# Optimization experiments

Hardware: AMD Instinct MI355X
Metric: run time of the kernel (lower is better)

Reference implementation:

```python
import jax, jax.numpy as jnp
import numpy as np

H, W = 768, 1024
N_ITER = 10
DIST_THR = 100.0 / 15.0
NORMAL_THR = 0.34
DAMP = 1e-9  # tiny ridge so the 6x6 normal-equation solve matches lstsq robustly


def _skew(w):
    z = jnp.zeros((), w.dtype)
    return jnp.stack([
        jnp.stack([z, -w[2], w[1]]),
        jnp.stack([w[2], z, -w[0]]),
        jnp.stack([-w[1], w[0], z]),
    ])


def _so3_exp(w):
    # Rodrigues formula, safe at w ~ 0
    th2 = jnp.dot(w, w)
    th = jnp.sqrt(th2 + 1e-12)
    Wm = _skew(w)
    return (jnp.eye(3, dtype=w.dtype)
            + (jnp.sin(th) / th) * Wm
            + ((1.0 - jnp.cos(th)) / (th2 + 1e-12)) * (Wm @ Wm))


def _pose(x):
    # lie_se3_to_SE3: rotation = exp(x[:3]), translation = x[3:]
    return _so3_exp(x[:3]), x[3:]


def _backproject(depth, K):
    # PointCloud.from_depth: grid_pts[v,u] = depth[v,u] * K^-1 @ [u, v, 1]
    vs, us = jnp.meshgrid(jnp.arange(H, dtype=depth.dtype),
                          jnp.arange(W, dtype=depth.dtype), indexing='ij')
    Kinv = jnp.linalg.inv(K)
    uv1 = jnp.stack([us, vs, jnp.ones_like(us)], axis=-1)  # [H,W,3]
    return (uv1 @ Kinv.T) * depth[..., None]               # [H,W,3]


def _grid_normals(pts):
    # normals from cross product of image-space gradients of the 3D grid
    du = jnp.gradient(pts, axis=1)
    dv = jnp.gradient(pts, axis=0)
    n = jnp.cross(du, dv)
    return n / jnp.sqrt(jnp.sum(n * n, axis=-1, keepdims=True) + 1e-12)


def _icp(ref_depth, target_pts, target_normals, K):
    dt = ref_depth.dtype
    ref_grid = _backproject(ref_depth, K)   # [H,W,3]
    ref_nrm = _grid_normals(ref_grid)       # [H,W,3]
    x = jnp.zeros(6, dtype=dt)
    cost = jnp.zeros((), dtype=dt)
    for _ in range(N_ITER):
        R, t = _pose(x)
        # transform target cloud into current ref camera frame: inv(T) @ p
        pts_c = (target_pts - t) @ R        # R^T (p - t), [N,3]
        nrm_c = target_normals @ R          # rotate normals by R^T
        # projective association
        uvw = pts_c @ K.T
        z = uvw[:, 2]
        zs = jnp.where(jnp.abs(z) > 1e-8, z, 1e-8)
        u = uvw[:, 0] / zs
        v = uvw[:, 1] / zs
        valid = (u > 0) & (u < W) & (v > 0) & (v < H) & (z > 1e-6)
        iu = jnp.clip(u, 0, W - 1).astype(jnp.int32)
        iv = jnp.clip(v, 0, H - 1).astype(jnp.int32)
        rg = ref_grid[iv, iu]               # gathered ref grid points [N,3]
        rn = ref_nrm[iv, iu]                # gathered ref grid normals [N,3]
        dist = jnp.sqrt(jnp.sum((rg - pts_c) ** 2, axis=-1) + 1e-12)
        valid = valid & (dist < DIST_THR) & (jnp.sum(rn * nrm_c, axis=-1) > NORMAL_THR)
        w = valid.astype(dt)
        # point-to-plane residual in world/target frame: n_trg . (T @ p_ref - p_trg)
        ref_world = rg @ R.T + t
        r = jnp.sum(target_normals * (ref_world - target_pts), axis=-1) * w
        # J row = n^T @ j_3d(p) = [cross(p, n), n]
        J = jnp.concatenate([jnp.cross(ref_world, target_normals), target_normals], axis=-1) * w[:, None]
        cost = jnp.sum(r * r) / jnp.maximum(jnp.sum(w), 1.0)
        A = J.T @ J + DAMP * jnp.eye(6, dtype=dt)
        x = x - jnp.linalg.solve(A, J.T @ r)  # Gauss-Newton step (= -lstsq(J, r))
    Rf, tf = _pose(x)
    T = jnp.eye(4, dtype=dt).at[:3, :3].set(Rf).at[:3, 3].set(tf)
    return T, cost


def setup_inputs() -> dict:
    key = jax.random.key(0)
    k1, k2 = jax.random.split(key)
    K = jnp.array([[1000.0, 0.0, 512.0],
                   [0.0, 1000.0, 384.0],
                   [0.0, 0.0, 1.0]], dtype=jnp.float32)
    vs, us = jnp.meshgrid(jnp.arange(H, dtype=jnp.float32),
                          jnp.arange(W, dtype=jnp.float32), indexing='ij')
    base = 1.0 + 0.2 * jnp.sin(vs / 47.0) * jnp.cos(us / 53.0)  # smooth surface
    ref_depth = (base + 0.001 * jax.random.normal(k1, (H, W))).astype(jnp.float32)
    trg_depth = (base + 0.001 * jax.random.normal(k2, (H, W))).astype(jnp.float32)
    tg = _backproject(trg_depth, K)
    tn = _grid_normals(tg)
    return {
        'ref_depth': ref_depth,
        'target_pts': tg.reshape(-1, 3),
        'target_normals': tn.reshape(-1, 3),
        'intrinsics': K,
    }


def reference(ref_depth, target_pts, target_normals, intrinsics):
    return _icp(ref_depth, target_pts, target_normals, intrinsics)
```

## Files before the change

kernel.cpp:

```cpp
#include <hip/hip_runtime.h>
#include <math.h>

#define H_IMG 768
#define W_IMG 1024
#define NPTS (H_IMG * W_IMG)
#define NITER 10
#define DIST_THR (100.0f / 15.0f)
#define NORMAL_THR 0.34f

struct Ctrl {
    double accum[NITER][32];
    double x[6];
    float  pose[NITER + 1][12];
    float  Kinv[9];
};

__global__ void setup_kernel(const float* __restrict__ K, Ctrl* c) {
    int tid = threadIdx.x;
    double* ac = &c->accum[0][0];
    for (int i = tid; i < NITER * 32; i += blockDim.x) ac[i] = 0.0;
    if (tid < 6) c->x[tid] = 0.0;
    if (tid == 0) {
        float* p0 = c->pose[0];
        p0[0] = 1.f; p0[1] = 0.f; p0[2] = 0.f;
        p0[3] = 0.f; p0[4] = 1.f; p0[5] = 0.f;
        p0[6] = 0.f; p0[7] = 0.f; p0[8] = 1.f;
        p0[9] = 0.f; p0[10] = 0.f; p0[11] = 0.f;
        double a = K[0], b = K[1], cc = K[2];
        double d = K[3], e = K[4], f = K[5];
        double g = K[6], h = K[7], i = K[8];
        double det = a * (e * i - f * h) - b * (d * i - f * g) + cc * (d * h - e * g);
        double idet = 1.0 / det;
        c->Kinv[0] = (float)((e * i - f * h) * idet);
        c->Kinv[1] = (float)((cc * h - b * i) * idet);
        c->Kinv[2] = (float)((b * f - cc * e) * idet);
        c->Kinv[3] = (float)((f * g - d * i) * idet);
        c->Kinv[4] = (float)((a * i - cc * g) * idet);
        c->Kinv[5] = (float)((cc * d - a * f) * idet);
        c->Kinv[6] = (float)((d * h - e * g) * idet);
        c->Kinv[7] = (float)((b * g - a * h) * idet);
        c->Kinv[8] = (float)((a * e - b * d) * idet);
    }
}

__global__ __launch_bounds__(256) void backproject_kernel(const float* __restrict__ depth,
                                                          const Ctrl* __restrict__ c,
                                                          float* __restrict__ grid) {
    int i = blockIdx.x * blockDim.x + threadIdx.x;
    if (i >= NPTS) return;
    int v = i >> 10;
    int u = i & 1023;
    float d = depth[i];
    float uf = (float)u, vf = (float)v;
    const float* Ki = c->Kinv;
    grid[3 * i + 0] = (Ki[0] * uf + Ki[1] * vf + Ki[2]) * d;
    grid[3 * i + 1] = (Ki[3] * uf + Ki[4] * vf + Ki[5]) * d;
    grid[3 * i + 2] = (Ki[6] * uf + Ki[7] * vf + Ki[8]) * d;
}

__global__ __launch_bounds__(256) void normals_kernel(const float* __restrict__ grid,
                                                      float* __restrict__ nrm) {
    int i = blockIdx.x * blockDim.x + threadIdx.x;
    if (i >= NPTS) return;
    int v = i >> 10;
    int u = i & 1023;
    int um = (u > 0) ? u - 1 : 0;
    int up = (u < W_IMG - 1) ? u + 1 : W_IMG - 1;
    int vm = (v > 0) ? v - 1 : 0;
    int vp = (v < H_IMG - 1) ? v + 1 : H_IMG - 1;
    float su = (u > 0 && u < W_IMG - 1) ? 0.5f : 1.0f;
    float sv = (v > 0 && v < H_IMG - 1) ? 0.5f : 1.0f;
    int il = (v * W_IMG + um) * 3, ir = (v * W_IMG + up) * 3;
    int it = (vm * W_IMG + u) * 3, ib = (vp * W_IMG + u) * 3;
    float dux = (grid[ir + 0] - grid[il + 0]) * su;
    float duy = (grid[ir + 1] - grid[il + 1]) * su;
    float duz = (grid[ir + 2] - grid[il + 2]) * su;
    float dvx = (grid[ib + 0] - grid[it + 0]) * sv;
    float dvy = (grid[ib + 1] - grid[it + 1]) * sv;
    float dvz = (grid[ib + 2] - grid[it + 2]) * sv;
    float nx = duy * dvz - duz * dvy;
    float ny = duz * dvx - dux * dvz;
    float nz = dux * dvy - duy * dvx;
    float len = sqrtf(nx * nx + ny * ny + nz * nz + 1e-12f);
    nrm[3 * i + 0] = nx / len;
    nrm[3 * i + 1] = ny / len;
    nrm[3 * i + 2] = nz / len;
}

__global__ __launch_bounds__(256) void icp_main(const float* __restrict__ tp,
                                                const float* __restrict__ tn,
                                                const float* __restrict__ grid,
                                                const float* __restrict__ nrm,
                                                const float* __restrict__ K,
                                                const float* __restrict__ pose,
                                                double* __restrict__ accum) {
    const float R0 = pose[0], R1 = pose[1], R2 = pose[2];
    const float R3 = pose[3], R4 = pose[4], R5 = pose[5];
    const float R6 = pose[6], R7 = pose[7], R8 = pose[8];
    const float t0 = pose[9], t1 = pose[10], t2 = pose[11];
    const float K0 = K[0], K1 = K[1], K2 = K[2];
    const float K3 = K[3], K4 = K[4], K5 = K[5];
    const float K6 = K[6], K7 = K[7], K8 = K[8];

    float acc[29];
#pragma unroll
    for (int k = 0; k < 29; ++k) acc[k] = 0.f;

    const int stride = gridDim.x * blockDim.x;
    for (int i = blockIdx.x * blockDim.x + threadIdx.x; i < NPTS; i += stride) {
        float p0 = tp[3 * i + 0], p1 = tp[3 * i + 1], p2 = tp[3 * i + 2];
        float n0 = tn[3 * i + 0], n1 = tn[3 * i + 1], n2 = tn[3 * i + 2];
        float d0 = p0 - t0, d1 = p1 - t1, d2 = p2 - t2;
        float pc0 = R0 * d0 + R3 * d1 + R6 * d2;
        float pc1 = R1 * d0 + R4 * d1 + R7 * d2;
        float pc2 = R2 * d0 + R5 * d1 + R8 * d2;
        float nc0 = R0 * n0 + R3 * n1 + R6 * n2;
        float nc1 = R1 * n0 + R4 * n1 + R7 * n2;
        float nc2 = R2 * n0 + R5 * n1 + R8 * n2;
        float uu = K0 * pc0 + K1 * pc1 + K2 * pc2;
        float vv = K3 * pc0 + K4 * pc1 + K5 * pc2;
        float zz = K6 * pc0 + K7 * pc1 + K8 * pc2;
        float zs = (fabsf(zz) > 1e-8f) ? zz : 1e-8f;
        float uf = uu / zs, vf = vv / zs;
        bool valid = (uf > 0.f) && (uf < (float)W_IMG) && (vf > 0.f) && (vf < (float)H_IMG) && (zz > 1e-6f);
        int iu = (int)fminf(fmaxf(uf, 0.f), (float)(W_IMG - 1));
        int iv = (int)fminf(fmaxf(vf, 0.f), (float)(H_IMG - 1));
        int gi = ((iv << 10) + iu) * 3;
        float rg0 = grid[gi + 0], rg1 = grid[gi + 1], rg2 = grid[gi + 2];
        float rn0 = nrm[gi + 0], rn1 = nrm[gi + 1], rn2 = nrm[gi + 2];
        float dd0 = rg0 - pc0, dd1 = rg1 - pc1, dd2 = rg2 - pc2;
        float dist = sqrtf(dd0 * dd0 + dd1 * dd1 + dd2 * dd2 + 1e-12f);
        valid = valid && (dist < DIST_THR) && (rn0 * nc0 + rn1 * nc1 + rn2 * nc2 > NORMAL_THR);
        if (valid) {
            float rw0 = R0 * rg0 + R1 * rg1 + R2 * rg2 + t0;
            float rw1 = R3 * rg0 + R4 * rg1 + R5 * rg2 + t1;
            float rw2 = R6 * rg0 + R7 * rg1 + R8 * rg2 + t2;
            float r = n0 * (rw0 - p0) + n1 * (rw1 - p1) + n2 * (rw2 - p2);
            float J[6];
            J[0] = rw1 * n2 - rw2 * n1;
            J[1] = rw2 * n0 - rw0 * n2;
            J[2] = rw0 * n1 - rw1 * n0;
            J[3] = n0; J[4] = n1; J[5] = n2;
            int cI = 0;
#pragma unroll
            for (int a = 0; a < 6; ++a) {
#pragma unroll
                for (int b = a; b < 6; ++b) acc[cI++] += J[a] * J[b];
            }
#pragma unroll
            for (int a = 0; a < 6; ++a) acc[21 + a] += J[a] * r;
            acc[27] += r * r;
            acc[28] += 1.f;
        }
    }

#pragma unroll
    for (int k = 0; k < 29; ++k) {
#pragma unroll
        for (int off = 32; off > 0; off >>= 1) acc[k] += __shfl_down(acc[k], off);
    }
    __shared__ float smem[4][29];
    int lane = threadIdx.x & 63;
    int wave = threadIdx.x >> 6;
    if (lane == 0) {
#pragma unroll
        for (int k = 0; k < 29; ++k) smem[wave][k] = acc[k];
    }
    __syncthreads();
    if (threadIdx.x < 29) {
        double s = (double)smem[0][threadIdx.x] + (double)smem[1][threadIdx.x]
                 + (double)smem[2][threadIdx.x] + (double)smem[3][threadIdx.x];
        atomicAdd(&accum[threadIdx.x], s);
    }
}

__global__ void icp_solve(Ctrl* c, const double* __restrict__ acc,
                          float* __restrict__ pose_next, float* __restrict__ out, int last) {
    if (threadIdx.x != 0 || blockIdx.x != 0) return;
    double M[6][7];
    int cI = 0;
    for (int a = 0; a < 6; ++a)
        for (int b = a; b < 6; ++b) {
            M[a][b] = acc[cI];
            M[b][a] = acc[cI];
            ++cI;
        }
    for (int a = 0; a < 6; ++a) M[a][6] = acc[21 + a];
    double cost = acc[27] / fmax(acc[28], 1.0);
    for (int d = 0; d < 6; ++d) M[d][d] += 1e-9;

    for (int col = 0; col < 6; ++col) {
        int piv = col;
        for (int r = col + 1; r < 6; ++r)
            if (fabs(M[r][col]) > fabs(M[piv][col])) piv = r;
        if (piv != col) {
            for (int k = col; k < 7; ++k) {
                double tmp = M[col][k]; M[col][k] = M[piv][k]; M[piv][k] = tmp;
            }
        }
        double p = M[col][col];
        for (int r = col + 1; r < 6; ++r) {
            double f = M[r][col] / p;
            for (int k = col; k < 7; ++k) M[r][k] -= f * M[col][k];
        }
    }
    double y[6];
    for (int i = 5; i >= 0; --i) {
        double s = M[i][6];
        for (int j = i + 1; j < 6; ++j) s -= M[i][j] * y[j];
        y[i] = s / M[i][i];
    }
    double xn[6];
    for (int i = 0; i < 6; ++i) {
        xn[i] = c->x[i] - y[i];
        c->x[i] = xn[i];
    }
    double wx = xn[0], wy = xn[1], wz = xn[2];
    double th2 = wx * wx + wy * wy + wz * wz;
    double th = sqrt(th2 + 1e-12);
    double sA = sin(th) / th;
    double sB = (1.0 - cos(th)) / (th2 + 1e-12);
    double R[9];
    R[0] = 1.0 + sB * (-(wy * wy + wz * wz));
    R[1] = sA * (-wz) + sB * (wx * wy);
    R[2] = sA * ( wy) + sB * (wx * wz);
    R[3] = sA * ( wz) + sB * (wx * wy);
    R[4] = 1.0 + sB * (-(wx * wx + wz * wz));
    R[5] = sA * (-wx) + sB * (wy * wz);
    R[6] = sA * (-wy) + sB * (wx * wz);
    R[7] = sA * ( wx) + sB * (wy * wz);
    R[8] = 1.0 + sB * (-(wx * wx + wy * wy));
    for (int k = 0; k < 9; ++k) pose_next[k] = (float)R[k];
    pose_next[9]  = (float)xn[3];
    pose_next[10] = (float)xn[4];
    pose_next[11] = (float)xn[5];
    if (last) {
        out[0]  = (float)R[0]; out[1]  = (float)R[1]; out[2]  = (float)R[2]; out[3]  = (float)xn[3];
        out[4]  = (float)R[3]; out[5]  = (float)R[4]; out[6]  = (float)R[5]; out[7]  = (float)xn[4];
        out[8]  = (float)R[6]; out[9]  = (float)R[7]; out[10] = (float)R[8]; out[11] = (float)xn[5];
        out[12] = 0.f; out[13] = 0.f; out[14] = 0.f; out[15] = 1.f;
        out[16] = (float)cost;
    }
}

extern "C" void kernel_launch(void* const* d_in, const int* in_sizes, int n_in,
                              void* d_out, int out_size, void* d_ws, size_t ws_size,
                              hipStream_t stream) {
    const float* ref_depth      = (const float*)d_in[0];
    const float* target_pts     = (const float*)d_in[1];
    const float* target_normals = (const float*)d_in[2];
    const float* K              = (const float*)d_in[3];
    float* out = (float*)d_out;
    char* ws = (char*)d_ws;

    const size_t grid_bytes = (size_t)NPTS * 3 * sizeof(float);
    float* ref_grid = (float*)ws;
    float* ref_nrm  = (float*)(ws + grid_bytes);
    Ctrl*  ctrl     = (Ctrl*)(ws + 2 * grid_bytes);

    setup_kernel<<<1, 256, 0, stream>>>(K, ctrl);
    backproject_kernel<<<NPTS / 256, 256, 0, stream>>>(ref_depth, ctrl, ref_grid);
    normals_kernel<<<NPTS / 256, 256, 0, stream>>>(ref_grid, ref_nrm);
    for (int it = 0; it < NITER; ++it) {
        icp_main<<<512, 256, 0, stream>>>(target_pts, target_normals, ref_grid, ref_nrm, K,
                                          ctrl->pose[it], &ctrl->accum[it][0]);
        icp_solve<<<1, 64, 0, stream>>>(ctrl, &ctrl->accum[it][0],
                                        ctrl->pose[it + 1], out, it == NITER - 1 ? 1 : 0);
    }
}
```

Before: 358.3 us.

## Fuse ICP into one cooperative persistent kernel with grid syncs

```diff
diff --git a/kernel.cpp b/kernel.cpp
--- a/kernel.cpp
+++ b/kernel.cpp
@@ -1,103 +1,102 @@
 #include <hip/hip_runtime.h>
+#include <hip/hip_cooperative_groups.h>
 #include <math.h>
+
+namespace cg = cooperative_groups;
 
 #define H_IMG 768
 #define W_IMG 1024
 #define NPTS (H_IMG * W_IMG)
 #define NITER 10
+#define NBLK 256
+#define NTHR 256
+#define TOTTHR (NBLK * NTHR)
+#define PPT (NPTS / TOTTHR)
 #define DIST_THR (100.0f / 15.0f)
 #define NORMAL_THR 0.34f
 
-struct Ctrl {
-    double accum[NITER][32];
-    double x[6];
-    float  pose[NITER + 1][12];
-    float  Kinv[9];
+struct SharedScratch {
+    float  smemF[4][29];
+    double smemD[4][29];
+    float  pose[12];
 };
 
-__global__ void setup_kernel(const float* __restrict__ K, Ctrl* c) {
-    int tid = threadIdx.x;
-    double* ac = &c->accum[0][0];
-    for (int i = tid; i < NITER * 32; i += blockDim.x) ac[i] = 0.0;
-    if (tid < 6) c->x[tid] = 0.0;
-    if (tid == 0) {
-        float* p0 = c->pose[0];
-        p0[0] = 1.f; p0[1] = 0.f; p0[2] = 0.f;
-        p0[3] = 0.f; p0[4] = 1.f; p0[5] = 0.f;
-        p0[6] = 0.f; p0[7] = 0.f; p0[8] = 1.f;
-        p0[9] = 0.f; p0[10] = 0.f; p0[11] = 0.f;
+__device__ __forceinline__ void dev_prep(int tid, const float* __restrict__ depth,
+                                         const float* __restrict__ K,
+                                         float* __restrict__ ref_grid,
+                                         float* __restrict__ ref_nrm) {
+    float Ki[9];
+    {
         double a = K[0], b = K[1], cc = K[2];
         double d = K[3], e = K[4], f = K[5];
         double g = K[6], h = K[7], i = K[8];
         double det = a * (e * i - f * h) - b * (d * i - f * g) + cc * (d * h - e * g);
         double idet = 1.0 / det;
-        c->Kinv[0] = (float)((e * i - f * h) * idet);
-        c->Kinv[1] = (float)((cc * h - b * i) * idet);
-        c->Kinv[2] = (float)((b * f - cc * e) * idet);
-        c->Kinv[3] = (float)((f * g - d * i) * idet);
-        c->Kinv[4] = (float)((a * i - cc * g) * idet);
-        c->Kinv[5] = (float)((cc * d - a * f) * idet);
-        c->Kinv[6] = (float)((d * h - e * g) * idet);
-        c->Kinv[7] = (float)((b * g - a * h) * idet);
-        c->Kinv[8] = (float)((a * e - b * d) * idet);
-    }
-}
-
-__global__ __launch_bounds__(256) void backproject_kernel(const float* __restrict__ depth,
-                                                          const Ctrl* __restrict__ c,
-                                                          float* __restrict__ grid) {
-    int i = blockIdx.x * blockDim.x + threadIdx.x;
-    if (i >= NPTS) return;
-    int v = i >> 10;
-    int u = i & 1023;
-    float d = depth[i];
-    float uf = (float)u, vf = (float)v;
-    const float* Ki = c->Kinv;
-    grid[3 * i + 0] = (Ki[0] * uf + Ki[1] * vf + Ki[2]) * d;
-    grid[3 * i + 1] = (Ki[3] * uf + Ki[4] * vf + Ki[5]) * d;
-    grid[3 * i + 2] = (Ki[6] * uf + Ki[7] * vf + Ki[8]) * d;
-}
-
-__global__ __launch_bounds__(256) void normals_kernel(const float* __restrict__ grid,
-                                                      float* __restrict__ nrm) {
-    int i = blockIdx.x * blockDim.x + threadIdx.x;
-    if (i >= NPTS) return;
-    int v = i >> 10;
-    int u = i & 1023;
-    int um = (u > 0) ? u - 1 : 0;
-    int up = (u < W_IMG - 1) ? u + 1 : W_IMG - 1;
-    int vm = (v > 0) ? v - 1 : 0;
-    int vp = (v < H_IMG - 1) ? v + 1 : H_IMG - 1;
-    float su = (u > 0 && u < W_IMG - 1) ? 0.5f : 1.0f;
-    float sv = (v > 0 && v < H_IMG - 1) ? 0.5f : 1.0f;
-    int il = (v * W_IMG + um) * 3, ir = (v * W_IMG + up) * 3;
-    int it = (vm * W_IMG + u) * 3, ib = (vp * W_IMG + u) * 3;
-    float dux = (grid[ir + 0] - grid[il + 0]) * su;
-    float duy = (grid[ir + 1] - grid[il + 1]) * su;
-    float duz = (grid[ir + 2] - grid[il + 2]) * su;
-    float dvx = (grid[ib + 0] - grid[it + 0]) * sv;
-    float dvy = (grid[ib + 1] - grid[it + 1]) * sv;
-    float dvz = (grid[ib + 2] - grid[it + 2]) * sv;
-    float nx = duy * dvz - duz * dvy;
-    float ny = duz * dvx - dux * dvz;
-    float nz = dux * dvy - duy * dvx;
-    float len = sqrtf(nx * nx + ny * ny + nz * nz + 1e-12f);
-    nrm[3 * i + 0] = nx / len;
-    nrm[3 * i + 1] = ny / len;
-    nrm[3 * i + 2] = nz / len;
-}
-
-__global__ __launch_bounds__(256) void icp_main(const float* __restrict__ tp,
-                                                const float* __restrict__ tn,
-                                                const float* __restrict__ grid,
-                                                const float* __restrict__ nrm,
-                                                const float* __restrict__ K,
-                                                const float* __restrict__ pose,
-                                                double* __restrict__ accum) {
-    const float R0 = pose[0], R1 = pose[1], R2 = pose[2];
-    const float R3 = pose[3], R4 = pose[4], R5 = pose[5];
-    const float R6 = pose[6], R7 = pose[7], R8 = pose[8];
-    const float t0 = pose[9], t1 = pose[10], t2 = pose[11];
+        Ki[0] = (float)((e * i - f * h) * idet);
+        Ki[1] = (float)((cc * h - b * i) * idet);
+        Ki[2] = (float)((b * f - cc * e) * idet);
+        Ki[3] = (float)((f * g - d * i) * idet);
+        Ki[4] = (float)((a * i - cc * g) * idet);
+        Ki[5] = (float)((cc * d - a * f) * idet);
+        Ki[6] = (float)((d * h - e * g) * idet);
+        Ki[7] = (float)((b * g - a * h) * idet);
+        Ki[8] = (float)((a * e - b * d) * idet);
+    }
+#pragma unroll
+    for (int q = 0; q < PPT; ++q) {
+        int p = tid + q * TOTTHR;
+        int v = p >> 10, u = p & 1023;
+        float uf = (float)u, vf = (float)v;
+        float d0 = depth[p];
+        float cx = (Ki[0] * uf + Ki[1] * vf + Ki[2]) * d0;
+        float cy = (Ki[3] * uf + Ki[4] * vf + Ki[5]) * d0;
+        float cz = (Ki[6] * uf + Ki[7] * vf + Ki[8]) * d0;
+        ref_grid[3 * p + 0] = cx;
+        ref_grid[3 * p + 1] = cy;
+        ref_grid[3 * p + 2] = cz;
+        int um = u > 0 ? u - 1 : 0, up = u < W_IMG - 1 ? u + 1 : W_IMG - 1;
+        int vm = v > 0 ? v - 1 : 0, vp = v < H_IMG - 1 ? v + 1 : H_IMG - 1;
+        float su = (u > 0 && u < W_IMG - 1) ? 0.5f : 1.0f;
+        float sv = (v > 0 && v < H_IMG - 1) ? 0.5f : 1.0f;
+        float dl = depth[v * W_IMG + um], dr = depth[v * W_IMG + up];
+        float dt = depth[vm * W_IMG + u], db = depth[vp * W_IMG + u];
+        float umf = (float)um, upf = (float)up, vmf = (float)vm, vpf = (float)vp;
+        float lx = (Ki[0] * umf + Ki[1] * vf + Ki[2]) * dl;
+        float ly = (Ki[3] * umf + Ki[4] * vf + Ki[5]) * dl;
+        float lz = (Ki[6] * umf + Ki[7] * vf + Ki[8]) * dl;
+        float rx = (Ki[0] * upf + Ki[1] * vf + Ki[2]) * dr;
+        float ry = (Ki[3] * upf + Ki[4] * vf + Ki[5]) * dr;
+        float rz = (Ki[6] * upf + Ki[7] * vf + Ki[8]) * dr;
+        float tx = (Ki[0] * uf + Ki[1] * vmf + Ki[2]) * dt;
+        float ty = (Ki[3] * uf + Ki[4] * vmf + Ki[5]) * dt;
+        float tz = (Ki[6] * uf + Ki[7] * vmf + Ki[8]) * dt;
+        float bx = (Ki[0] * uf + Ki[1] * vpf + Ki[2]) * db;
+        float by = (Ki[3] * uf + Ki[4] * vpf + Ki[5]) * db;
+        float bz = (Ki[6] * uf + Ki[7] * vpf + Ki[8]) * db;
+        float dux = (rx - lx) * su, duy = (ry - ly) * su, duz = (rz - lz) * su;
+        float dvx = (bx - tx) * sv, dvy = (by - ty) * sv, dvz = (bz - tz) * sv;
+        float nx = duy * dvz - duz * dvy;
+        float ny = duz * dvx - dux * dvz;
+        float nz = dux * dvy - duy * dvx;
+        float il = 1.0f / sqrtf(nx * nx + ny * ny + nz * nz + 1e-12f);
+        ref_nrm[3 * p + 0] = nx * il;
+        ref_nrm[3 * p + 1] = ny * il;
+        ref_nrm[3 * p + 2] = nz * il;
+    }
+}
+
+__device__ __forceinline__ void dev_sweep(int tid,
+                                          const float* __restrict__ tp,
+                                          const float* __restrict__ tn,
+                                          const float* __restrict__ grid,
+                                          const float* __restrict__ nrm,
+                                          const float* __restrict__ K,
+                                          float* __restrict__ partial_row,
+                                          SharedScratch* sh) {
+    const float R0 = sh->pose[0], R1 = sh->pose[1], R2 = sh->pose[2];
+    const float R3 = sh->pose[3], R4 = sh->pose[4], R5 = sh->pose[5];
+    const float R6 = sh->pose[6], R7 = sh->pose[7], R8 = sh->pose[8];
+    const float t0 = sh->pose[9], t1 = sh->pose[10], t2 = sh->pose[11];
     const float K0 = K[0], K1 = K[1], K2 = K[2];
     const float K3 = K[3], K4 = K[4], K5 = K[5];
     const float K6 = K[6], K7 = K[7], K8 = K[8];
@@ -106,8 +105,8 @@
 #pragma unroll
     for (int k = 0; k < 29; ++k) acc[k] = 0.f;
 
-    const int stride = gridDim.x * blockDim.x;
-    for (int i = blockIdx.x * blockDim.x + threadIdx.x; i < NPTS; i += stride) {
+    for (int q = 0; q < PPT; ++q) {
+        int i = tid + q * TOTTHR;
         float p0 = tp[3 * i + 0], p1 = tp[3 * i + 1], p2 = tp[3 * i + 2];
         float n0 = tn[3 * i + 0], n1 = tn[3 * i + 1], n2 = tn[3 * i + 2];
         float d0 = p0 - t0, d1 = p1 - t1, d2 = p2 - t2;
@@ -143,10 +142,9 @@
             J[3] = n0; J[4] = n1; J[5] = n2;
             int cI = 0;
 #pragma unroll
-            for (int a = 0; a < 6; ++a) {
+            for (int a = 0; a < 6; ++a)
 #pragma unroll
                 for (int b = a; b < 6; ++b) acc[cI++] += J[a] * J[b];
-            }
 #pragma unroll
             for (int a = 0; a < 6; ++a) acc[21 + a] += J[a] * r;
             acc[27] += r * r;
@@ -159,88 +157,183 @@
 #pragma unroll
         for (int off = 32; off > 0; off >>= 1) acc[k] += __shfl_down(acc[k], off);
     }
-    __shared__ float smem[4][29];
-    int lane = threadIdx.x & 63;
-    int wave = threadIdx.x >> 6;
+    int lane = threadIdx.x & 63, wv = threadIdx.x >> 6;
     if (lane == 0) {
 #pragma unroll
-        for (int k = 0; k < 29; ++k) smem[wave][k] = acc[k];
+        for (int k = 0; k < 29; ++k) sh->smemF[wv][k] = acc[k];
     }
     __syncthreads();
     if (threadIdx.x < 29) {
-        double s = (double)smem[0][threadIdx.x] + (double)smem[1][threadIdx.x]
-                 + (double)smem[2][threadIdx.x] + (double)smem[3][threadIdx.x];
-        atomicAdd(&accum[threadIdx.x], s);
-    }
-}
-
-__global__ void icp_solve(Ctrl* c, const double* __restrict__ acc,
-                          float* __restrict__ pose_next, float* __restrict__ out, int last) {
-    if (threadIdx.x != 0 || blockIdx.x != 0) return;
-    double M[6][7];
-    int cI = 0;
-    for (int a = 0; a < 6; ++a)
-        for (int b = a; b < 6; ++b) {
-            M[a][b] = acc[cI];
-            M[b][a] = acc[cI];
-            ++cI;
-        }
-    for (int a = 0; a < 6; ++a) M[a][6] = acc[21 + a];
-    double cost = acc[27] / fmax(acc[28], 1.0);
-    for (int d = 0; d < 6; ++d) M[d][d] += 1e-9;
-
-    for (int col = 0; col < 6; ++col) {
-        int piv = col;
-        for (int r = col + 1; r < 6; ++r)
-            if (fabs(M[r][col]) > fabs(M[piv][col])) piv = r;
-        if (piv != col) {
-            for (int k = col; k < 7; ++k) {
-                double tmp = M[col][k]; M[col][k] = M[piv][k]; M[piv][k] = tmp;
+        partial_row[threadIdx.x] = sh->smemF[0][threadIdx.x] + sh->smemF[1][threadIdx.x] +
+                                   sh->smemF[2][threadIdx.x] + sh->smemF[3][threadIdx.x];
+    }
+}
+
+__device__ __forceinline__ void dev_reduce_solve(const float* __restrict__ partials,
+                                                 double* x, SharedScratch* sh,
+                                                 float* __restrict__ out_final) {
+    double a2[29];
+    const float* row = partials + threadIdx.x * 32;
+#pragma unroll
+    for (int k = 0; k < 29; ++k) a2[k] = (double)row[k];
+#pragma unroll
+    for (int k = 0; k < 29; ++k) {
+#pragma unroll
+        for (int off = 32; off > 0; off >>= 1) a2[k] += __shfl_down(a2[k], off);
+    }
+    int lane = threadIdx.x & 63, wv = threadIdx.x >> 6;
+    if (lane == 0) {
+#pragma unroll
+        for (int k = 0; k < 29; ++k) sh->smemD[wv][k] = a2[k];
+    }
+    __syncthreads();
+    if (threadIdx.x == 0) {
+        double T[29];
+#pragma unroll
+        for (int k = 0; k < 29; ++k)
+            T[k] = sh->smemD[0][k] + sh->smemD[1][k] + sh->smemD[2][k] + sh->smemD[3][k];
+        double M[6][7];
+        int cI = 0;
+#pragma unroll
+        for (int a = 0; a < 6; ++a)
+#pragma unroll
+            for (int b = a; b < 6; ++b) { M[a][b] = T[cI]; M[b][a] = T[cI]; ++cI; }
+#pragma unroll
+        for (int a = 0; a < 6; ++a) M[a][6] = T[21 + a];
+        double cost = T[27] / fmax(T[28], 1.0);
+#pragma unroll
+        for (int d = 0; d < 6; ++d) M[d][d] += 1e-9;
+#pragma unroll
+        for (int col = 0; col < 6; ++col) {
+            double ip = 1.0 / M[col][col];
+#pragma unroll
+            for (int r = col + 1; r < 6; ++r) {
+                double f = M[r][col] * ip;
+#pragma unroll
+                for (int k = col; k < 7; ++k) M[r][k] -= f * M[col][k];
             }
         }
-        double p = M[col][col];
-        for (int r = col + 1; r < 6; ++r) {
-            double f = M[r][col] / p;
-            for (int k = col; k < 7; ++k) M[r][k] -= f * M[col][k];
-        }
-    }
-    double y[6];
-    for (int i = 5; i >= 0; --i) {
-        double s = M[i][6];
-        for (int j = i + 1; j < 6; ++j) s -= M[i][j] * y[j];
-        y[i] = s / M[i][i];
-    }
-    double xn[6];
-    for (int i = 0; i < 6; ++i) {
-        xn[i] = c->x[i] - y[i];
-        c->x[i] = xn[i];
-    }
-    double wx = xn[0], wy = xn[1], wz = xn[2];
-    double th2 = wx * wx + wy * wy + wz * wz;
-    double th = sqrt(th2 + 1e-12);
-    double sA = sin(th) / th;
-    double sB = (1.0 - cos(th)) / (th2 + 1e-12);
-    double R[9];
-    R[0] = 1.0 + sB * (-(wy * wy + wz * wz));
-    R[1] = sA * (-wz) + sB * (wx * wy);
-    R[2] = sA * ( wy) + sB * (wx * wz);
-    R[3] = sA * ( wz) + sB * (wx * wy);
-    R[4] = 1.0 + sB * (-(wx * wx + wz * wz));
-    R[5] = sA * (-wx) + sB * (wy * wz);
-    R[6] = sA * (-wy) + sB * (wx * wz);
-    R[7] = sA * ( wx) + sB * (wy * wz);
-    R[8] = 1.0 + sB * (-(wx * wx + wy * wy));
-    for (int k = 0; k < 9; ++k) pose_next[k] = (float)R[k];
-    pose_next[9]  = (float)xn[3];
-    pose_next[10] = (float)xn[4];
-    pose_next[11] = (float)xn[5];
-    if (last) {
-        out[0]  = (float)R[0]; out[1]  = (float)R[1]; out[2]  = (float)R[2]; out[3]  = (float)xn[3];
-        out[4]  = (float)R[3]; out[5]  = (float)R[4]; out[6]  = (float)R[5]; out[7]  = (float)xn[4];
-        out[8]  = (float)R[6]; out[9]  = (float)R[7]; out[10] = (float)R[8]; out[11] = (float)xn[5];
-        out[12] = 0.f; out[13] = 0.f; out[14] = 0.f; out[15] = 1.f;
-        out[16] = (float)cost;
-    }
+        double y[6];
+#pragma unroll
+        for (int i2 = 5; i2 >= 0; --i2) {
+            double s = M[i2][6];
+#pragma unroll
+            for (int j = i2 + 1; j < 6; ++j) s -= M[i2][j] * y[j];
+            y[i2] = s / M[i2][i2];
+        }
+#pragma unroll
+        for (int k = 0; k < 6; ++k) x[k] -= y[k];
+        double th2 = x[0] * x[0] + x[1] * x[1] + x[2] * x[2];
+        double th = sqrt(th2 + 1e-12);
+        double sA = sin(th) / th;
+        double sB = (1.0 - cos(th)) / (th2 + 1e-12);
+        double R[9];
+        R[0] = 1.0 + sB * (-(x[1] * x[1] + x[2] * x[2]));
+        R[1] = sA * (-x[2]) + sB * (x[0] * x[1]);
+        R[2] = sA * ( x[1]) + sB * (x[0] * x[2]);
+        R[3] = sA * ( x[2]) + sB * (x[0] * x[1]);
+        R[4] = 1.0 + sB * (-(x[0] * x[0] + x[2] * x[2]));
+        R[5] = sA * (-x[0]) + sB * (x[1] * x[2]);
+        R[6] = sA * (-x[1]) + sB * (x[0] * x[2]);
+        R[7] = sA * ( x[0]) + sB * (x[1] * x[2]);
+        R[8] = 1.0 + sB * (-(x[0] * x[0] + x[1] * x[1]));
+#pragma unroll
+        for (int k = 0; k < 9; ++k) sh->pose[k] = (float)R[k];
+        sh->pose[9] = (float)x[3]; sh->pose[10] = (float)x[4]; sh->pose[11] = (float)x[5];
+        if (out_final) {
+            out_final[0]  = (float)R[0]; out_final[1]  = (float)R[1]; out_final[2]  = (float)R[2]; out_final[3]  = (float)x[3];
+            out_final[4]  = (float)R[3]; out_final[5]  = (float)R[4]; out_final[6]  = (float)R[5]; out_final[7]  = (float)x[4];
+            out_final[8]  = (float)R[6]; out_final[9]  = (float)R[7]; out_final[10] = (float)R[8]; out_final[11] = (float)x[5];
+            out_final[12] = 0.f; out_final[13] = 0.f; out_final[14] = 0.f; out_final[15] = 1.f;
+            out_final[16] = (float)cost;
+        }
+    }
+}
+
+__global__ __launch_bounds__(NTHR) void icp_coop(const float* __restrict__ depth,
+                                                 const float* __restrict__ tp,
+                                                 const float* __restrict__ tn,
+                                                 const float* __restrict__ K,
+                                                 float* __restrict__ out,
+                                                 float* __restrict__ ref_grid,
+                                                 float* __restrict__ ref_nrm,
+                                                 float* __restrict__ part0,
+                                                 float* __restrict__ part1) {
+    __shared__ SharedScratch sh;
+    cg::grid_group gg = cg::this_grid();
+    const int tid = blockIdx.x * NTHR + threadIdx.x;
+    dev_prep(tid, depth, K, ref_grid, ref_nrm);
+    double x[6] = {0, 0, 0, 0, 0, 0};
+    gg.sync();
+    for (int it = 0; it < NITER; ++it) {
+        float* pout = (it & 1) ? part1 : part0;
+        const float* pprev = (it & 1) ? part0 : part1;
+        if (it == 0) {
+            if (threadIdx.x == 0) {
+                sh.pose[0] = 1.f; sh.pose[1] = 0.f; sh.pose[2] = 0.f;
+                sh.pose[3] = 0.f; sh.pose[4] = 1.f; sh.pose[5] = 0.f;
+                sh.pose[6] = 0.f; sh.pose[7] = 0.f; sh.pose[8] = 1.f;
+                sh.pose[9] = 0.f; sh.pose[10] = 0.f; sh.pose[11] = 0.f;
+            }
+        } else {
+            dev_reduce_solve(pprev, x, &sh, nullptr);
+        }
+        __syncthreads();
+        dev_sweep(tid, tp, tn, ref_grid, ref_nrm, K, pout + blockIdx.x * 32, &sh);
+        gg.sync();
+    }
+    if (blockIdx.x == 0) {
+        dev_reduce_solve(part1, x, &sh, out);
+    }
+}
+
+__global__ __launch_bounds__(NTHR) void k_prep(const float* __restrict__ depth,
+                                               const float* __restrict__ K,
+                                               float* __restrict__ ref_grid,
+                                               float* __restrict__ ref_nrm) {
+    dev_prep(blockIdx.x * NTHR + threadIdx.x, depth, K, ref_grid, ref_nrm);
+}
+
+__global__ __launch_bounds__(NTHR) void k_iter(int it, const float* __restrict__ pprev,
+                                               float* __restrict__ pout, double* __restrict__ xbuf,
+                                               const float* __restrict__ tp, const float* __restrict__ tn,
+                                               const float* __restrict__ grid, const float* __restrict__ nrm,
+                                               const float* __restrict__ K) {
+    __shared__ SharedScratch sh;
+    double x[6] = {0, 0, 0, 0, 0, 0};
+    if (it == 0) {
+        if (threadIdx.x == 0) {
+            sh.pose[0] = 1.f; sh.pose[1] = 0.f; sh.pose[2] = 0.f;
+            sh.pose[3] = 0.f; sh.pose[4] = 1.f; sh.pose[5] = 0.f;
+            sh.pose[6] = 0.f; sh.pose[7] = 0.f; sh.pose[8] = 1.f;
+            sh.pose[9] = 0.f; sh.pose[10] = 0.f; sh.pose[11] = 0.f;
+        }
+    } else {
+        if (threadIdx.x == 0) {
+#pragma unroll
+            for (int k = 0; k < 6; ++k) x[k] = xbuf[k];
+        }
+        dev_reduce_solve(pprev, x, &sh, nullptr);
+    }
+    if (threadIdx.x == 0 && blockIdx.x == 0) {
+#pragma unroll
+        for (int k = 0; k < 6; ++k) xbuf[k] = x[k];
+    }
+    __syncthreads();
+    dev_sweep(blockIdx.x * NTHR + threadIdx.x, tp, tn, grid, nrm, K,
+              pout + blockIdx.x * 32, &sh);
+}
+
+__global__ __launch_bounds__(NTHR) void k_final(const float* __restrict__ pprev,
+                                                double* __restrict__ xbuf,
+                                                float* __restrict__ out) {
+    __shared__ SharedScratch sh;
+    double x[6] = {0, 0, 0, 0, 0, 0};
+    if (threadIdx.x == 0) {
+#pragma unroll
+        for (int k = 0; k < 6; ++k) x[k] = xbuf[k];
+    }
+    dev_reduce_solve(pprev, x, &sh, out);
 }
 
 extern "C" void kernel_launch(void* const* d_in, const int* in_sizes, int n_in,
@@ -254,17 +347,26 @@
     char* ws = (char*)d_ws;
 
     const size_t grid_bytes = (size_t)NPTS * 3 * sizeof(float);
-    float* ref_grid = (float*)ws;
-    float* ref_nrm  = (float*)(ws + grid_bytes);
-    Ctrl*  ctrl     = (Ctrl*)(ws + 2 * grid_bytes);
-
-    setup_kernel<<<1, 256, 0, stream>>>(K, ctrl);
-    backproject_kernel<<<NPTS / 256, 256, 0, stream>>>(ref_depth, ctrl, ref_grid);
-    normals_kernel<<<NPTS / 256, 256, 0, stream>>>(ref_grid, ref_nrm);
-    for (int it = 0; it < NITER; ++it) {
-        icp_main<<<512, 256, 0, stream>>>(target_pts, target_normals, ref_grid, ref_nrm, K,
-                                          ctrl->pose[it], &ctrl->accum[it][0]);
-        icp_solve<<<1, 64, 0, stream>>>(ctrl, &ctrl->accum[it][0],
-                                        ctrl->pose[it + 1], out, it == NITER - 1 ? 1 : 0);
-    }
-}
+    float*  ref_grid = (float*)ws;
+    float*  ref_nrm  = (float*)(ws + grid_bytes);
+    float*  part0    = (float*)(ws + 2 * grid_bytes);
+    float*  part1    = (float*)(ws + 2 * grid_bytes + (size_t)NBLK * 32 * sizeof(float));
+    double* xbuf     = (double*)(ws + 2 * grid_bytes + 2 * (size_t)NBLK * 32 * sizeof(float));
+
+    void* args[] = {
+        (void*)&ref_depth, (void*)&target_pts, (void*)&target_normals, (void*)&K,
+        (void*)&out, (void*)&ref_grid, (void*)&ref_nrm, (void*)&part0, (void*)&part1
+    };
+    hipError_t err = hipLaunchCooperativeKernel((const void*)icp_coop,
+                                                dim3(NBLK), dim3(NTHR), args, 0, stream);
+    if (err != hipSuccess) {
+        k_prep<<<NBLK, NTHR, 0, stream>>>(ref_depth, K, ref_grid, ref_nrm);
+        float* pp[2] = { part0, part1 };
+        for (int it = 0; it < NITER; ++it) {
+            const float* pprev = (it == 0) ? part1 : pp[(it - 1) & 1];
+            k_iter<<<NBLK, NTHR, 0, stream>>>(it, pprev, pp[it & 1], xbuf,
+                                              target_pts, target_normals, ref_grid, ref_nrm, K);
+        }
+        k_final<<<1, NTHR, 0, stream>>>(pp[(NITER - 1) & 1], xbuf, out);
+    }
+}
```

Result: slower. 609.3 us (+70.1%).
